# Performance work log

Hardware: AMD Instinct MI355X
Metric: run time of the kernel (lower is better)

Reference implementation:

```python
import jax, jax.numpy as jnp
import numpy as np
import math

B, N, M, O = 64, 2048, 64, 128  # batch, neurons, in_dims, out_dims


def setup_inputs() -> dict:
    key = jax.random.key(0)
    kx, kw, kb = jax.random.split(key, 3)
    s = 1.0 / math.sqrt(M + O)
    x = jax.random.normal(kx, (B, N, M), dtype=jnp.float32)
    # master weights fp32, init U(-s, s) as in the torch module
    w1 = jax.random.uniform(kw, (M, O, N), dtype=jnp.float32, minval=-s, maxval=s)
    b1 = jnp.zeros((1, N, O), dtype=jnp.float32)
    return {"x": x, "w1": w1, "b1": b1}


def reference(x, w1, b1):
    # N independent per-neuron linears: [B,N,M] x [M,O,N] -> [B,N,O]
    # cast master weights/bias to compute dtype (matches .to(x.dtype))
    w = w1.astype(x.dtype)
    b = b1.astype(x.dtype)
    return jnp.einsum('bnm,mon->bno', x, w) + b
```

## Files before the change

kernel.cpp:

```cpp
#include <hip/hip_runtime.h>
#include <hip/hip_bf16.h>

#define B_DIM 64
#define N_TOT 2048
#define M_DIM 64
#define O_DIM 128
#define NT 8

typedef __bf16 bf16x8 __attribute__((ext_vector_type(8)));
typedef float f32x4 __attribute__((ext_vector_type(4)));

__device__ __forceinline__ unsigned short f2bf(float f) {
    union { float f; unsigned int u; } v;
    v.f = f;
    unsigned int r = v.u + 0x7fffu + ((v.u >> 16) & 1u);
    return (unsigned short)(r >> 16);
}

__global__ __launch_bounds__(512, 2) void superlinear_mfma(
    const float* __restrict__ x, const float* __restrict__ w1,
    const float* __restrict__ b1, float* __restrict__ out)
{
    __shared__ unsigned char wlds[NT * O_DIM * M_DIM * 2];

    const int tid  = threadIdx.x;
    const int lane = tid & 63;
    const int wave = tid >> 6;

    const int bid  = blockIdx.x;
    const int nblk = (bid & 7) * 32 + (bid >> 3);
    const int n0   = nblk * NT;

    #pragma unroll
    for (int it = 0; it < 8; ++it) {
        int u  = it * 512 + tid;
        int n4 = u & 1;
        int o  = (u >> 1) & 127;
        int mq = u >> 8;
        int m  = mq * 4;
        const float* gp = w1 + ((size_t)m * O_DIM + o) * N_TOT + n0 + n4 * 4;
        float4 r0 = *(const float4*)(gp);
        float4 r1 = *(const float4*)(gp + (size_t)O_DIM * N_TOT);
        float4 r2 = *(const float4*)(gp + (size_t)2 * O_DIM * N_TOT);
        float4 r3 = *(const float4*)(gp + (size_t)3 * O_DIM * N_TOT);
        const float* a0 = (const float*)&r0;
        const float* a1 = (const float*)&r1;
        const float* a2 = (const float*)&r2;
        const float* a3 = (const float*)&r3;
        #pragma unroll
        for (int j = 0; j < 4; ++j) {
            int nn = n4 * 4 + j;
            unsigned short e0 = f2bf(a0[j]);
            unsigned short e1 = f2bf(a1[j]);
            unsigned short e2 = f2bf(a2[j]);
            unsigned short e3 = f2bf(a3[j]);
            unsigned long long pk =
                (unsigned long long)e0 | ((unsigned long long)e1 << 16) |
                ((unsigned long long)e2 << 32) | ((unsigned long long)e3 << 48);
            unsigned addr = (unsigned)(nn * (O_DIM * M_DIM * 2) + o * (M_DIM * 2) + m * 2);
            addr ^= (unsigned)((o & 7) << 4);
            *(unsigned long long*)(wlds + addr) = pk;
        }
    }
    __syncthreads();

    const int nn  = wave;
    const int n   = n0 + nn;
    const int col = lane & 15;
    const int kg  = lane >> 4;

    f32x4 acc[4][8];
    #pragma unroll
    for (int ot = 0; ot < 8; ++ot) {
        float bv = b1[(size_t)n * O_DIM + ot * 16 + col];
        #pragma unroll
        for (int bt = 0; bt < 4; ++bt) {
            acc[bt][ot][0] = bv; acc[bt][ot][1] = bv;
            acc[bt][ot][2] = bv; acc[bt][ot][3] = bv;
        }
    }

    #pragma unroll
    for (int kc = 0; kc < 2; ++kc) {
        bf16x8 af[4];
        #pragma unroll
        for (int bt = 0; bt < 4; ++bt) {
            int b = bt * 16 + col;
            const float* xp = x + ((size_t)b * N_TOT + n) * M_DIM + kc * 32 + kg * 8;
            float4 lo = *(const float4*)xp;
            float4 hi = *(const float4*)(xp + 4);
            const float* lp = (const float*)&lo;
            const float* hp = (const float*)&hi;
            union { bf16x8 v; unsigned short s[8]; } cvt;
            #pragma unroll
            for (int j = 0; j < 4; ++j) { cvt.s[j] = f2bf(lp[j]); cvt.s[4 + j] = f2bf(hp[j]); }
            af[bt] = cvt.v;
        }
        #pragma unroll
        for (int ot = 0; ot < 8; ++ot) {
            unsigned addr = (unsigned)(nn * 16384 + (ot * 16 + col) * 128 + kc * 64 + kg * 16);
            addr ^= (unsigned)((col & 7) << 4);
            bf16x8 bfrag = *(const bf16x8*)(wlds + addr);
            #pragma unroll
            for (int bt = 0; bt < 4; ++bt)
                acc[bt][ot] = __builtin_amdgcn_mfma_f32_16x16x32_bf16(af[bt], bfrag, acc[bt][ot], 0, 0, 0);
        }
    }

    #pragma unroll
    for (int bt = 0; bt < 4; ++bt) {
        #pragma unroll
        for (int r = 0; r < 4; ++r) {
            int b = bt * 16 + kg * 4 + r;
            float* op = out + ((size_t)b * N_TOT + n) * O_DIM + col;
            #pragma unroll
            for (int ot = 0; ot < 8; ++ot)
                op[ot * 16] = acc[bt][ot][r];
        }
    }
}

extern "C" void kernel_launch(void* const* d_in, const int* in_sizes, int n_in,
                              void* d_out, int out_size, void* d_ws, size_t ws_size,
                              hipStream_t stream) {
    const float* x  = (const float*)d_in[0];
    const float* w1 = (const float*)d_in[1];
    const float* b1 = (const float*)d_in[2];
    float* out = (float*)d_out;
    superlinear_mfma<<<dim3(256), dim3(512), 0, stream>>>(x, w1, b1, out);
}
```

Baseline: 35.55 us.

## Split batch across two blocks and stage weights in two K-chunks

Each block now processes half the batch, doubling the grid, and stages the bf16-converted weights into LDS in two K-halves with a matching swizzle. This halves LDS use and accumulator registers, so launch bounds allow more blocks per CU and more parallelism. Bias is added in the epilogue instead of initializing accumulators. The trade-off is that each weight tile is read twice from global memory and extra barriers serialize staging and compute.

```diff
diff --git a/kernel.cpp b/kernel.cpp
--- a/kernel.cpp
+++ b/kernel.cpp
@@ -17,75 +17,33 @@
     return (unsigned short)(r >> 16);
 }
 
-__global__ __launch_bounds__(512, 2) void superlinear_mfma(
+__global__ __launch_bounds__(512, 4) void superlinear_mfma(
     const float* __restrict__ x, const float* __restrict__ w1,
     const float* __restrict__ b1, float* __restrict__ out)
 {
-    __shared__ unsigned char wlds[NT * O_DIM * M_DIM * 2];
+    __shared__ unsigned char wlds[NT * O_DIM * 32 * 2];
 
     const int tid  = threadIdx.x;
     const int lane = tid & 63;
     const int wave = tid >> 6;
 
     const int bid  = blockIdx.x;
-    const int nblk = (bid & 7) * 32 + (bid >> 3);
+    const int swz  = (bid & 7) * 64 + (bid >> 3);
+    const int nblk = swz >> 1;
+    const int bh   = swz & 1;
     const int n0   = nblk * NT;
-
-    #pragma unroll
-    for (int it = 0; it < 8; ++it) {
-        int u  = it * 512 + tid;
-        int n4 = u & 1;
-        int o  = (u >> 1) & 127;
-        int mq = u >> 8;
-        int m  = mq * 4;
-        const float* gp = w1 + ((size_t)m * O_DIM + o) * N_TOT + n0 + n4 * 4;
-        float4 r0 = *(const float4*)(gp);
-        float4 r1 = *(const float4*)(gp + (size_t)O_DIM * N_TOT);
-        float4 r2 = *(const float4*)(gp + (size_t)2 * O_DIM * N_TOT);
-        float4 r3 = *(const float4*)(gp + (size_t)3 * O_DIM * N_TOT);
-        const float* a0 = (const float*)&r0;
-        const float* a1 = (const float*)&r1;
-        const float* a2 = (const float*)&r2;
-        const float* a3 = (const float*)&r3;
-        #pragma unroll
-        for (int j = 0; j < 4; ++j) {
-            int nn = n4 * 4 + j;
-            unsigned short e0 = f2bf(a0[j]);
-            unsigned short e1 = f2bf(a1[j]);
-            unsigned short e2 = f2bf(a2[j]);
-            unsigned short e3 = f2bf(a3[j]);
-            unsigned long long pk =
-                (unsigned long long)e0 | ((unsigned long long)e1 << 16) |
-                ((unsigned long long)e2 << 32) | ((unsigned long long)e3 << 48);
-            unsigned addr = (unsigned)(nn * (O_DIM * M_DIM * 2) + o * (M_DIM * 2) + m * 2);
-            addr ^= (unsigned)((o & 7) << 4);
-            *(unsigned long long*)(wlds + addr) = pk;
-        }
-    }
-    __syncthreads();
 
     const int nn  = wave;
     const int n   = n0 + nn;
     const int col = lane & 15;
     const int kg  = lane >> 4;
 
-    f32x4 acc[4][8];
-    #pragma unroll
-    for (int ot = 0; ot < 8; ++ot) {
-        float bv = b1[(size_t)n * O_DIM + ot * 16 + col];
-        #pragma unroll
-        for (int bt = 0; bt < 4; ++bt) {
-            acc[bt][ot][0] = bv; acc[bt][ot][1] = bv;
-            acc[bt][ot][2] = bv; acc[bt][ot][3] = bv;
-        }
-    }
-
+    bf16x8 af[2][2];
     #pragma unroll
     for (int kc = 0; kc < 2; ++kc) {
-        bf16x8 af[4];
         #pragma unroll
-        for (int bt = 0; bt < 4; ++bt) {
-            int b = bt * 16 + col;
+        for (int bt = 0; bt < 2; ++bt) {
+            int b = bh * 32 + bt * 16 + col;
             const float* xp = x + ((size_t)b * N_TOT + n) * M_DIM + kc * 32 + kg * 8;
             float4 lo = *(const float4*)xp;
             float4 hi = *(const float4*)(xp + 4);
@@ -94,28 +52,85 @@
             union { bf16x8 v; unsigned short s[8]; } cvt;
             #pragma unroll
             for (int j = 0; j < 4; ++j) { cvt.s[j] = f2bf(lp[j]); cvt.s[4 + j] = f2bf(hp[j]); }
-            af[bt] = cvt.v;
-        }
-        #pragma unroll
-        for (int ot = 0; ot < 8; ++ot) {
-            unsigned addr = (unsigned)(nn * 16384 + (ot * 16 + col) * 128 + kc * 64 + kg * 16);
-            addr ^= (unsigned)((col & 7) << 4);
-            bf16x8 bfrag = *(const bf16x8*)(wlds + addr);
-            #pragma unroll
-            for (int bt = 0; bt < 4; ++bt)
-                acc[bt][ot] = __builtin_amdgcn_mfma_f32_16x16x32_bf16(af[bt], bfrag, acc[bt][ot], 0, 0, 0);
+            af[kc][bt] = cvt.v;
         }
     }
 
+    f32x4 acc[2][8];
     #pragma unroll
-    for (int bt = 0; bt < 4; ++bt) {
+    for (int bt = 0; bt < 2; ++bt)
+        #pragma unroll
+        for (int ot = 0; ot < 8; ++ot)
+            acc[bt][ot] = (f32x4)0.0f;
+
+    auto stage = [&](int kc) {
+        #pragma unroll
+        for (int it = 0; it < 4; ++it) {
+            int u  = it * 512 + tid;
+            int n4 = u & 1;
+            int o  = (u >> 1) & 127;
+            int kq = (u >> 8) & 7;
+            int kl = kq * 4;
+            const float* gp = w1 + ((size_t)(kc * 32 + kl) * O_DIM + o) * N_TOT + n0 + n4 * 4;
+            float4 r0 = *(const float4*)(gp);
+            float4 r1 = *(const float4*)(gp + (size_t)O_DIM * N_TOT);
+            float4 r2 = *(const float4*)(gp + (size_t)2 * O_DIM * N_TOT);
+            float4 r3 = *(const float4*)(gp + (size_t)3 * O_DIM * N_TOT);
+            const float* a0 = (const float*)&r0;
+            const float* a1 = (const float*)&r1;
+            const float* a2 = (const float*)&r2;
+            const float* a3 = (const float*)&r3;
+            #pragma unroll
+            for (int j = 0; j < 4; ++j) {
+                int nnw = n4 * 4 + j;
+                unsigned short e0 = f2bf(a0[j]);
+                unsigned short e1 = f2bf(a1[j]);
+                unsigned short e2 = f2bf(a2[j]);
+                unsigned short e3 = f2bf(a3[j]);
+                unsigned long long pk =
+                    (unsigned long long)e0 | ((unsigned long long)e1 << 16) |
+                    ((unsigned long long)e2 << 32) | ((unsigned long long)e3 << 48);
+                unsigned addr = (unsigned)(nnw * 4096 + o * 32 + kl) * 2u;
+                addr ^= ((unsigned)(o >> 1) & 3u) << 4;
+                *(unsigned long long*)(wlds + addr) = pk;
+            }
+        }
+    };
+
+    auto compute = [&](int kc) {
+        #pragma unroll
+        for (int ot = 0; ot < 8; ++ot) {
+            unsigned addr = (unsigned)(nn * 8192 + (ot * 16 + col) * 64 + kg * 16);
+            addr ^= ((unsigned)(col >> 1) & 3u) << 4;
+            bf16x8 bfrag = *(const bf16x8*)(wlds + addr);
+            #pragma unroll
+            for (int bt = 0; bt < 2; ++bt)
+                acc[bt][ot] = __builtin_amdgcn_mfma_f32_16x16x32_bf16(af[kc][bt], bfrag, acc[bt][ot], 0, 0, 0);
+        }
+    };
+
+    stage(0);
+    __syncthreads();
+    compute(0);
+    __syncthreads();
+    stage(1);
+    __syncthreads();
+    compute(1);
+
+    float bv[8];
+    #pragma unroll
+    for (int ot = 0; ot < 8; ++ot)
+        bv[ot] = b1[(size_t)n * O_DIM + ot * 16 + col];
+
+    #pragma unroll
+    for (int bt = 0; bt < 2; ++bt) {
         #pragma unroll
         for (int r = 0; r < 4; ++r) {
-            int b = bt * 16 + kg * 4 + r;
+            int b = bh * 32 + bt * 16 + kg * 4 + r;
             float* op = out + ((size_t)b * N_TOT + n) * O_DIM + col;
             #pragma unroll
             for (int ot = 0; ot < 8; ++ot)
-                op[ot * 16] = acc[bt][ot][r];
+                op[ot * 16] = acc[bt][ot][r] + bv[ot];
         }
     }
 }
@@ -127,5 +142,5 @@
     const float* w1 = (const float*)d_in[1];
     const float* b1 = (const float*)d_in[2];
     float* out = (float*)d_out;
-    superlinear_mfma<<<dim3(256), dim3(512), 0, stream>>>(x, w1, b1, out);
+    superlinear_mfma<<<dim3(512), dim3(512), 0, stream>>>(x, w1, b1, out);
 }
```

Result: slower. 40.06 us (+12.7%).
